# Optimization experiments

Measured on AMD Instinct MI355X. Metric: run time of the kernel, lower is better.

The kernel has to match this reference:

```python
import jax, jax.numpy as jnp
import numpy as np

B, T, D = 4, 2048, 2048
P, K, ALPHA, R = 512, 16, 4, 32
E_RATIO = 0.8
EPS = 1e-6


def rmsnorm(x, g):
    return x * jax.lax.rsqrt(jnp.mean(x * x, axis=-1, keepdims=True) + EPS) * g


def dale_signs():
    # first e_ratio*P neurons excitatory (+1), rest inhibitory (-1)
    return jnp.where(jnp.arange(P) < int(E_RATIO * P), 1.0, -1.0)


def quant_dale(w, signs):
    # STE sign-quantization with per-neuron mean-abs scale + Dale's-law sign constraint
    scale = jnp.mean(jnp.abs(w), axis=-1, keepdims=True)  # [P,1]
    q = scale * signs[:, None] * jnp.ones_like(w)         # magnitude=scale, sign fixed per neuron
    return w + jax.lax.stop_gradient(q - w)


def synapse_graph(x, idx, w):
    # x: [B,T,D], idx: [P,K] int, w: [P,K] -> dendritic inputs [B,T,P,K]
    return jnp.take(x, idx, axis=-1) * w


def perceptron(x_dend, Wp, Wout, signs):
    Wq = quant_dale(Wp, signs)                              # [P,K]
    u = jnp.einsum('btpk,pk->btp', x_dend, Wq)              # [B,T,P]
    f = jax.nn.sigmoid(u)                                   # gate [B,T,P]
    f_out = quant_dale(Wout, signs)                         # [P,ALPHA]
    y = (f * u)[..., None] * f_out                          # [B,T,P,ALPHA]
    return u, f, y, f_out


def low_rank_ssm(t, f, s0, U, V, Wgate, bgate):
    # t,f: [B,T,P]; s0: [B,R]. Low-rank gated linear scan in R dims.
    z = jnp.einsum('btp,pr->btr', t, U)
    lam = jax.nn.sigmoid(jnp.einsum('btp,pr->btr', f, Wgate) + bgate)

    def step(s, inp):
        z_t, l_t = inp
        s = l_t * s + z_t
        return s, s

    sT, S = jax.lax.scan(step, s0, (jnp.moveaxis(z, 1, 0), jnp.moveaxis(lam, 1, 0)))
    tilde = jnp.einsum('btr,rp->btp', jnp.moveaxis(S, 0, 1), V)
    return tilde, sT


def flatten_ports(y):
    return y.reshape(*y.shape[:-2], P * ALPHA)


def setup_inputs() -> dict:
    key = jax.random.key(0)
    ks = jax.random.split(key, 14)
    sc = 0.1
    return {
        'x': jax.random.normal(ks[0], (B, T, D), jnp.float32),
        'state': jnp.zeros((B, R), jnp.float32),
        'g1': jnp.ones((D,), jnp.float32),
        'g2': jnp.ones((D,), jnp.float32),
        'idx_ssm': jax.random.randint(ks[1], (P, K), 0, D),
        'wg_ssm': jax.random.normal(ks[2], (P, K), jnp.float32) * sc,
        'idx_mlp': jax.random.randint(ks[3], (P, K), 0, D),
        'wg_mlp': jax.random.normal(ks[4], (P, K), jnp.float32) * sc,
        'Wp_ssm': jax.random.normal(ks[5], (P, K), jnp.float32) * sc,
        'Wout_ssm': jax.random.normal(ks[6], (P, ALPHA), jnp.float32) * sc,
        'Wp_mlp': jax.random.normal(ks[7], (P, K), jnp.float32) * sc,
        'Wout_mlp': jax.random.normal(ks[8], (P, ALPHA), jnp.float32) * sc,
        'U': jax.random.normal(ks[9], (P, R), jnp.float32) * sc,
        'V': jax.random.normal(ks[10], (R, P), jnp.float32) * sc,
        'Wgate': jax.random.normal(ks[11], (P, R), jnp.float32) * sc,
        'bgate': jnp.zeros((R,), jnp.float32),
    }


def reference(x, state, g1, g2, idx_ssm, wg_ssm, idx_mlp, wg_mlp,
              Wp_ssm, Wout_ssm, Wp_mlp, Wout_mlp, U, V, Wgate, bgate):
    signs = dale_signs()
    # --- SSM branch ---
    h1 = rmsnorm(x, g1)
    x_dend_ssm = synapse_graph(h1, idx_ssm, wg_ssm)
    u_ssm, f_ssm, _, f_out = perceptron(x_dend_ssm, Wp_ssm, Wout_ssm, signs)
    t_ssm = f_ssm * u_ssm
    tilde_t, new_state = low_rank_ssm(t_ssm, f_ssm, state, U, V, Wgate, bgate)
    y_ssm = (f_ssm * tilde_t)[..., None] * f_out            # [B,T,P,ALPHA]
    x_after = x + flatten_ports(y_ssm)
    # --- MLP branch ---
    h2 = rmsnorm(x_after, g2)
    x_dend_mlp = synapse_graph(h2, idx_mlp, wg_mlp)
    _, _, y_mlp, _ = perceptron(x_dend_mlp, Wp_mlp, Wout_mlp, signs)
    x_out = x_after + flatten_ports(y_mlp)
    return x_out, new_state
```

## Files before the change

### kernel.cpp

```cpp
#include <hip/hip_runtime.h>
#include <hip/hip_bf16.h>

#define B_ 4
#define T_ 2048
#define D_ 2048
#define P_ 512
#define K_ 16
#define ALPHA_ 4
#define R_ 32
#define NE_ 409
#define EPS_ 1e-6f
#define G_ 4

typedef unsigned short u16;
typedef unsigned int u32;

__device__ __forceinline__ float sigmoidf_(float x) {
  return 1.0f / (1.0f + __expf(-x));
}
__device__ __forceinline__ float bfb2f(u32 u) {
  return __uint_as_float(u << 16);
}
__device__ __forceinline__ u16 f2bfb(float f) {
  __hip_bfloat16 h = __float2bfloat16(f);
  return *reinterpret_cast<u16*>(&h);
}

__global__ __launch_bounds__(256, 4) void k_phase1(
    const float* __restrict__ x, const float* __restrict__ g1,
    const int* __restrict__ idx, const float* __restrict__ wg,
    const float* __restrict__ U, const float* __restrict__ Wgt,
    const float* __restrict__ bg, const float* __restrict__ Wp,
    u16* __restrict__ f_ssm, float* __restrict__ z, float* __restrict__ lam) {
  __shared__ u16 h1[G_][D_];
  __shared__ u32 ft[G_][P_];
  __shared__ float red[G_][4];
  __shared__ float zp[G_][R_][4];
  __shared__ float lp[G_][R_][4];

  int tid = threadIdx.x;
  int token0 = blockIdx.x * G_;
  int b = token0 >> 11;
  int t0 = token0 & (T_ - 1);
  int p0 = 2 * tid, p1 = p0 + 1;

  float xv[G_][8];
#pragma unroll
  for (int tok = 0; tok < G_; tok++) {
    const float4* xp = reinterpret_cast<const float4*>(x + (size_t)(token0 + tok) * D_ + tid * 8);
    *reinterpret_cast<float4*>(&xv[tok][0]) = xp[0];
    *reinterpret_cast<float4*>(&xv[tok][4]) = xp[1];
  }
  float gv[8];
  {
    const float4* gp = reinterpret_cast<const float4*>(g1 + tid * 8);
    *reinterpret_cast<float4*>(&gv[0]) = gp[0];
    *reinterpret_cast<float4*>(&gv[4]) = gp[1];
  }
  float wq0, wq1;
  {
    const float4* w0 = reinterpret_cast<const float4*>(Wp + p0 * K_);
    const float4* w1 = reinterpret_cast<const float4*>(Wp + p1 * K_);
    float a0 = 0, a1 = 0;
#pragma unroll
    for (int q = 0; q < 4; q++) {
      float4 v0 = w0[q], v1 = w1[q];
      a0 += fabsf(v0.x) + fabsf(v0.y) + fabsf(v0.z) + fabsf(v0.w);
      a1 += fabsf(v1.x) + fabsf(v1.y) + fabsf(v1.z) + fabsf(v1.w);
    }
    wq0 = ((p0 < NE_) ? 1.0f : -1.0f) * a0 * (1.0f / K_);
    wq1 = ((p1 < NE_) ? 1.0f : -1.0f) * a1 * (1.0f / K_);
  }

#pragma unroll
  for (int tok = 0; tok < G_; tok++) {
    float s = 0;
#pragma unroll
    for (int i = 0; i < 8; i++) s += xv[tok][i] * xv[tok][i];
#pragma unroll
    for (int off = 32; off; off >>= 1) s += __shfl_down(s, off);
    if ((tid & 63) == 0) red[tok][tid >> 6] = s;
  }
  __syncthreads();
#pragma unroll
  for (int tok = 0; tok < G_; tok++) {
    float inv = rsqrtf((red[tok][0] + red[tok][1] + red[tok][2] + red[tok][3]) * (1.0f / D_) + EPS_);
    u16 tmp[8];
#pragma unroll
    for (int i = 0; i < 8; i++) tmp[i] = f2bfb(xv[tok][i] * inv * gv[i]);
    *reinterpret_cast<uint4*>(&h1[tok][tid * 8]) = *reinterpret_cast<const uint4*>(tmp);
  }

  union { int4 v[4]; int s[16]; } iu0, iu1;
  union { float4 v[4]; float s[16]; } wu0, wu1;
  {
    const int4* ip0 = reinterpret_cast<const int4*>(idx + p0 * K_);
    const int4* ip1 = reinterpret_cast<const int4*>(idx + p1 * K_);
    const float4* wp0 = reinterpret_cast<const float4*>(wg + p0 * K_);
    const float4* wp1 = reinterpret_cast<const float4*>(wg + p1 * K_);
#pragma unroll
    for (int q = 0; q < 4; q++) { iu0.v[q] = ip0[q]; iu1.v[q] = ip1[q]; wu0.v[q] = wp0[q]; wu1.v[q] = wp1[q]; }
  }
  __syncthreads();

#pragma unroll
  for (int tok = 0; tok < G_; tok++) {
    float a0 = 0, a1 = 0;
#pragma unroll
    for (int k = 0; k < K_; k++) {
      a0 += bfb2f(h1[tok][iu0.s[k]]) * wu0.s[k];
      a1 += bfb2f(h1[tok][iu1.s[k]]) * wu1.s[k];
    }
    float u0 = wq0 * a0, u1 = wq1 * a1;
    float f0 = sigmoidf_(u0), f1 = sigmoidf_(u1);
    u32 pk0 = (u32)f2bfb(f0) | ((u32)f2bfb(f0 * u0) << 16);
    u32 pk1 = (u32)f2bfb(f1) | ((u32)f2bfb(f1 * u1) << 16);
    *reinterpret_cast<uint2*>(&ft[tok][p0]) = make_uint2(pk0, pk1);
    *reinterpret_cast<u32*>(f_ssm + (size_t)(token0 + tok) * P_ + p0) =
        (u32)f2bfb(f0) | ((u32)f2bfb(f1) << 16);
  }
  __syncthreads();

  int r = tid & 31, g = tid >> 5;
  float zs[G_], ls[G_];
#pragma unroll
  for (int tok = 0; tok < G_; tok++) { zs[tok] = 0; ls[tok] = 0; }
  int pbase = g * 64;
#pragma unroll 8
  for (int pp = 0; pp < 64; pp++) {
    int p = pbase + pp;
    float uu = U[p * R_ + r];
    float ww = Wgt[p * R_ + r];
#pragma unroll
    for (int tok = 0; tok < G_; tok++) {
      u32 v = ft[tok][p];
      zs[tok] += bfb2f(v >> 16) * uu;
      ls[tok] += bfb2f(v & 0xffffu) * ww;
    }
  }
#pragma unroll
  for (int tok = 0; tok < G_; tok++) {
    zs[tok] += __shfl_down(zs[tok], 32);
    ls[tok] += __shfl_down(ls[tok], 32);
  }
  int wid = tid >> 6;
  if ((tid & 63) < 32) {
#pragma unroll
    for (int tok = 0; tok < G_; tok++) {
      zp[tok][r][wid] = zs[tok];
      lp[tok][r][wid] = ls[tok];
    }
  }
  __syncthreads();
  if (tid < R_) {
    float bgr = bg[tid];
    float z4[G_], l4[G_];
#pragma unroll
    for (int tok = 0; tok < G_; tok++) {
      float zz = zp[tok][tid][0] + zp[tok][tid][1] + zp[tok][tid][2] + zp[tok][tid][3];
      float ll = lp[tok][tid][0] + lp[tok][tid][1] + lp[tok][tid][2] + lp[tok][tid][3];
      z4[tok] = zz;
      l4[tok] = sigmoidf_(ll + bgr);
    }
    size_t o = ((size_t)(b * R_ + tid)) * T_ + t0;
    *reinterpret_cast<float4*>(&z[o]) = *reinterpret_cast<const float4*>(z4);
    *reinterpret_cast<float4*>(&lam[o]) = *reinterpret_cast<const float4*>(l4);
  }
}

__global__ __launch_bounds__(64) void k_scan(
    const float* __restrict__ z, const float* __restrict__ lam,
    const float* __restrict__ state, float* __restrict__ S,
    float* __restrict__ out_state) {
  int br = blockIdx.x;
  int lane = threadIdx.x;
  const float* zr = z + (size_t)br * T_ + lane * 32;
  const float* lr = lam + (size_t)br * T_ + lane * 32;
  float zb[32], lb[32];
#pragma unroll
  for (int i = 0; i < 32; i += 4) {
    *reinterpret_cast<float4*>(&zb[i]) = *reinterpret_cast<const float4*>(&zr[i]);
    *reinterpret_cast<float4*>(&lb[i]) = *reinterpret_cast<const float4*>(&lr[i]);
  }
  float A = 1.0f, Z = 0.0f;
#pragma unroll
  for (int i = 0; i < 32; i++) { Z = lb[i] * Z + zb[i]; A *= lb[i]; }
  for (int off = 1; off < 64; off <<= 1) {
    float Ap = __shfl_up(A, off);
    float Zp = __shfl_up(Z, off);
    if (lane >= off) { Z = A * Zp + Z; A = A * Ap; }
  }
  float s0 = state[br];
  float Ae = __shfl_up(A, 1);
  float Ze = __shfl_up(Z, 1);
  float s = (lane == 0) ? s0 : (Ae * s0 + Ze);
  float sb[32];
#pragma unroll
  for (int i = 0; i < 32; i++) { s = lb[i] * s + zb[i]; sb[i] = s; }
  float* Sr = S + (size_t)br * T_ + lane * 32;
#pragma unroll
  for (int i = 0; i < 32; i += 4)
    *reinterpret_cast<float4*>(&Sr[i]) = *reinterpret_cast<const float4*>(&sb[i]);
  if (lane == 63) out_state[br] = s;
}

__global__ __launch_bounds__(256, 4) void k_phase3(
    const float* __restrict__ x, const float* __restrict__ g2,
    const int* __restrict__ idx, const float* __restrict__ wg,
    const float* __restrict__ V, const float* __restrict__ S,
    const u16* __restrict__ f_ssm, const float* __restrict__ Wo_s,
    const float* __restrict__ Wp_m, const float* __restrict__ Wo_m,
    float* __restrict__ out) {
  __shared__ float Sl[G_][R_];
  __shared__ u16 h2[G_][D_];
  __shared__ float red[G_][4];

  int tid = threadIdx.x;
  int token0 = blockIdx.x * G_;
  int b = token0 >> 11;
  int t0 = token0 & (T_ - 1);
  int p0 = 2 * tid, p1 = p0 + 1;

  if (tid < G_ * R_) {
    int tok = tid >> 5, r = tid & 31;
    Sl[tok][r] = S[((size_t)(b * R_ + r)) * T_ + t0 + tok];
  }

  float xa[G_][8];
#pragma unroll
  for (int tok = 0; tok < G_; tok++) {
    const float4* xp = reinterpret_cast<const float4*>(x + (size_t)(token0 + tok) * D_ + tid * 8);
    *reinterpret_cast<float4*>(&xa[tok][0]) = xp[0];
    *reinterpret_cast<float4*>(&xa[tok][4]) = xp[1];
  }
  u32 fpair[G_];
#pragma unroll
  for (int tok = 0; tok < G_; tok++)
    fpair[tok] = *reinterpret_cast<const u32*>(f_ssm + (size_t)(token0 + tok) * P_ + p0);

  float sgn0 = (p0 < NE_) ? 1.0f : -1.0f;
  float sgn1 = (p1 < NE_) ? 1.0f : -1.0f;
  float fo_s0, fo_s1, fo_m0, fo_m1, wq_m0, wq_m1;
  {
    float4 a = *reinterpret_cast<const float4*>(Wo_s + p0 * ALPHA_);
    float4 c = *reinterpret_cast<const float4*>(Wo_s + p1 * ALPHA_);
    fo_s0 = sgn0 * (fabsf(a.x) + fabsf(a.y) + fabsf(a.z) + fabsf(a.w)) * (1.0f / ALPHA_);
    fo_s1 = sgn1 * (fabsf(c.x) + fabsf(c.y) + fabsf(c.z) + fabsf(c.w)) * (1.0f / ALPHA_);
    float4 e = *reinterpret_cast<const float4*>(Wo_m + p0 * ALPHA_);
    float4 g = *reinterpret_cast<const float4*>(Wo_m + p1 * ALPHA_);
    fo_m0 = sgn0 * (fabsf(e.x) + fabsf(e.y) + fabsf(e.z) + fabsf(e.w)) * (1.0f / ALPHA_);
    fo_m1 = sgn1 * (fabsf(g.x) + fabsf(g.y) + fabsf(g.z) + fabsf(g.w)) * (1.0f / ALPHA_);
    const float4* w0 = reinterpret_cast<const float4*>(Wp_m + p0 * K_);
    const float4* w1 = reinterpret_cast<const float4*>(Wp_m + p1 * K_);
    float a0 = 0, a1 = 0;
#pragma unroll
    for (int q = 0; q < 4; q++) {
      float4 v0 = w0[q], v1 = w1[q];
      a0 += fabsf(v0.x) + fabsf(v0.y) + fabsf(v0.z) + fabsf(v0.w);
      a1 += fabsf(v1.x) + fabsf(v1.y) + fabsf(v1.z) + fabsf(v1.w);
    }
    wq_m0 = sgn0 * a0 * (1.0f / K_);
    wq_m1 = sgn1 * a1 * (1.0f / K_);
  }
  float gv[8];
  {
    const float4* gp = reinterpret_cast<const float4*>(g2 + tid * 8);
    *reinterpret_cast<float4*>(&gv[0]) = gp[0];
    *reinterpret_cast<float4*>(&gv[4]) = gp[1];
  }
  __syncthreads();

  float til0[G_], til1[G_];
#pragma unroll
  for (int tok = 0; tok < G_; tok++) { til0[tok] = 0; til1[tok] = 0; }
#pragma unroll 8
  for (int r = 0; r < R_; r++) {
    float2 vv = *reinterpret_cast<const float2*>(V + r * P_ + p0);
#pragma unroll
    for (int tok = 0; tok < G_; tok++) {
      float s = Sl[tok][r];
      til0[tok] += s * vv.x;
      til1[tok] += s * vv.y;
    }
  }

#pragma unroll
  for (int tok = 0; tok < G_; tok++) {
    float f0 = bfb2f(fpair[tok] & 0xffffu);
    float f1 = bfb2f(fpair[tok] >> 16);
    float val0 = f0 * til0[tok] * fo_s0;
    float val1 = f1 * til1[tok] * fo_s1;
    float ss = 0;
#pragma unroll
    for (int a = 0; a < 4; a++) {
      xa[tok][a] += val0;
      xa[tok][4 + a] += val1;
      ss += xa[tok][a] * xa[tok][a] + xa[tok][4 + a] * xa[tok][4 + a];
    }
#pragma unroll
    for (int off = 32; off; off >>= 1) ss += __shfl_down(ss, off);
    if ((tid & 63) == 0) red[tok][tid >> 6] = ss;
  }
  __syncthreads();
#pragma unroll
  for (int tok = 0; tok < G_; tok++) {
    float inv = rsqrtf((red[tok][0] + red[tok][1] + red[tok][2] + red[tok][3]) * (1.0f / D_) + EPS_);
    u16 tmp[8];
#pragma unroll
    for (int i = 0; i < 8; i++) tmp[i] = f2bfb(xa[tok][i] * inv * gv[i]);
    *reinterpret_cast<uint4*>(&h2[tok][tid * 8]) = *reinterpret_cast<const uint4*>(tmp);
  }
  __syncthreads();

#pragma unroll
  for (int j = 0; j < 2; j++) {
    int p = p0 + j;
    union { int4 v[4]; int s[16]; } iu;
    union { float4 v[4]; float s[16]; } wu;
    const int4* ip = reinterpret_cast<const int4*>(idx + p * K_);
    const float4* wp = reinterpret_cast<const float4*>(wg + p * K_);
#pragma unroll
    for (int q = 0; q < 4; q++) { iu.v[q] = ip[q]; wu.v[q] = wp[q]; }
    float wqm = j ? wq_m1 : wq_m0;
    float fom = j ? fo_m1 : fo_m0;
#pragma unroll
    for (int tok = 0; tok < G_; tok++) {
      float acc = 0;
#pragma unroll
      for (int k = 0; k < K_; k++) acc += bfb2f(h2[tok][iu.s[k]]) * wu.s[k];
      float u = wqm * acc;
      float f = sigmoidf_(u);
      float val = f * u * fom;
#pragma unroll
      for (int a = 0; a < 4; a++) xa[tok][j * 4 + a] += val;
    }
  }
#pragma unroll
  for (int tok = 0; tok < G_; tok++) {
    float4* op = reinterpret_cast<float4*>(out + (size_t)(token0 + tok) * D_ + tid * 8);
    op[0] = *reinterpret_cast<const float4*>(&xa[tok][0]);
    op[1] = *reinterpret_cast<const float4*>(&xa[tok][4]);
  }
}

extern "C" void kernel_launch(void* const* d_in, const int* in_sizes, int n_in,
                              void* d_out, int out_size, void* d_ws, size_t ws_size,
                              hipStream_t stream) {
  const float* x     = (const float*)d_in[0];
  const float* state = (const float*)d_in[1];
  const float* g1    = (const float*)d_in[2];
  const float* g2    = (const float*)d_in[3];
  const int*   idx_s = (const int*)d_in[4];
  const float* wg_s  = (const float*)d_in[5];
  const int*   idx_m = (const int*)d_in[6];
  const float* wg_m  = (const float*)d_in[7];
  const float* Wp_s  = (const float*)d_in[8];
  const float* Wo_s  = (const float*)d_in[9];
  const float* Wp_m  = (const float*)d_in[10];
  const float* Wo_m  = (const float*)d_in[11];
  const float* U     = (const float*)d_in[12];
  const float* V     = (const float*)d_in[13];
  const float* Wgt   = (const float*)d_in[14];
  const float* bg    = (const float*)d_in[15];
  float* out = (float*)d_out;

  char* ws = (char*)d_ws;
  u16* f_ssm = (u16*)ws;
  size_t off = (size_t)B_ * T_ * P_ * 2;
  float* z   = (float*)(ws + off); off += (size_t)B_ * R_ * T_ * 4;
  float* lam = (float*)(ws + off); off += (size_t)B_ * R_ * T_ * 4;
  float* S   = (float*)(ws + off);

  hipLaunchKernelGGL(k_phase1, dim3(B_ * T_ / G_), dim3(256), 0, stream,
                     x, g1, idx_s, wg_s, U, Wgt, bg, Wp_s, f_ssm, z, lam);
  hipLaunchKernelGGL(k_scan, dim3(B_ * R_), dim3(64), 0, stream,
                     z, lam, state, S, out + (size_t)B_ * T_ * D_);
  hipLaunchKernelGGL(k_phase3, dim3(B_ * T_ / G_), dim3(256), 0, stream,
                     x, g2, idx_m, wg_m, V, S, f_ssm, Wo_s, Wp_m, Wo_m, out);
}
```

Measured before the change: 254.4 us.

## Fuse three kernels into one cooperative persistent kernel with grid syncs

Replaces the three separate launches (phase1, scan, phase3) with a single cooperative kernel that loops over token groups persistently and uses grid.sync between phases, falling back to the three-kernel path if the cooperative launch fails. The aim is to remove launch gaps and tail effects between phases. It also hand-rolls the bf16 rounding, moves the idx/wg loads before a sync, and merges phase3's two per-neuron gather loops into one. The risks are grid-wide barrier cost, the scan phase using only 128 blocks while the rest idle, and occupancy limits of the persistent grid.

```diff
diff --git a/kernel.cpp b/kernel.cpp
--- a/kernel.cpp
+++ b/kernel.cpp
@@ -1,5 +1,8 @@
 #include <hip/hip_runtime.h>
 #include <hip/hip_bf16.h>
+#include <hip/hip_cooperative_groups.h>
+
+namespace cg = cooperative_groups;
 
 #define B_ 4
 #define T_ 2048
@@ -11,6 +14,7 @@
 #define NE_ 409
 #define EPS_ 1e-6f
 #define G_ 4
+#define NGRP_ (B_ * T_ / G_)
 
 typedef unsigned short u16;
 typedef unsigned int u32;
@@ -22,45 +26,80 @@
   return __uint_as_float(u << 16);
 }
 __device__ __forceinline__ u16 f2bfb(float f) {
-  __hip_bfloat16 h = __float2bfloat16(f);
-  return *reinterpret_cast<u16*>(&h);
-}
-
-__global__ __launch_bounds__(256, 4) void k_phase1(
+  u32 bits = __float_as_uint(f);
+  u32 lsb = (bits >> 16) & 1u;
+  bits += 0x7fffu + lsb;
+  return (u16)(bits >> 16);
+}
+
+struct SmemP1 {
+  u16 h[G_ * D_];
+  u32 ftw[G_ * P_];
+  float zp[G_][R_][4];
+  float lp[G_][R_][4];
+  float red[G_][4];
+};
+struct SmemP3 {
+  u16 h[G_ * D_];
+  float Sl[G_][R_];
+  float red[G_][4];
+};
+union SmemU { SmemP1 p1; SmemP3 p3; };
+
+__device__ __forceinline__ void phase1_dev(
+    SmemP1& sm, int gi, int tid,
     const float* __restrict__ x, const float* __restrict__ g1,
-    const int* __restrict__ idx, const float* __restrict__ wg,
-    const float* __restrict__ U, const float* __restrict__ Wgt,
-    const float* __restrict__ bg, const float* __restrict__ Wp,
-    u16* __restrict__ f_ssm, float* __restrict__ z, float* __restrict__ lam) {
-  __shared__ u16 h1[G_][D_];
-  __shared__ u32 ft[G_][P_];
-  __shared__ float red[G_][4];
-  __shared__ float zp[G_][R_][4];
-  __shared__ float lp[G_][R_][4];
-
-  int tid = threadIdx.x;
-  int token0 = blockIdx.x * G_;
+    const int* __restrict__ idx_s, const float* __restrict__ wg_s,
+    const float* __restrict__ Wp_s, const float* __restrict__ U,
+    const float* __restrict__ Wgt, const float* __restrict__ bg,
+    u32* __restrict__ ftg, float* __restrict__ z, float* __restrict__ lam) {
+  int token0 = gi * G_;
   int b = token0 >> 11;
   int t0 = token0 & (T_ - 1);
   int p0 = 2 * tid, p1 = p0 + 1;
 
+  float gv[8];
+  {
+    const float4* gp = reinterpret_cast<const float4*>(g1 + tid * 8);
+    *reinterpret_cast<float4*>(&gv[0]) = gp[0];
+    *reinterpret_cast<float4*>(&gv[4]) = gp[1];
+  }
   float xv[G_][8];
 #pragma unroll
   for (int tok = 0; tok < G_; tok++) {
     const float4* xp = reinterpret_cast<const float4*>(x + (size_t)(token0 + tok) * D_ + tid * 8);
     *reinterpret_cast<float4*>(&xv[tok][0]) = xp[0];
     *reinterpret_cast<float4*>(&xv[tok][4]) = xp[1];
-  }
-  float gv[8];
-  {
-    const float4* gp = reinterpret_cast<const float4*>(g1 + tid * 8);
-    *reinterpret_cast<float4*>(&gv[0]) = gp[0];
-    *reinterpret_cast<float4*>(&gv[4]) = gp[1];
+    float ss = 0;
+#pragma unroll
+    for (int i = 0; i < 8; i++) ss += xv[tok][i] * xv[tok][i];
+#pragma unroll
+    for (int off = 32; off; off >>= 1) ss += __shfl_down(ss, off);
+    if ((tid & 63) == 0) sm.red[tok][tid >> 6] = ss;
+  }
+  __syncthreads();
+#pragma unroll
+  for (int tok = 0; tok < G_; tok++) {
+    float inv = rsqrtf((sm.red[tok][0] + sm.red[tok][1] + sm.red[tok][2] + sm.red[tok][3]) * (1.0f / D_) + EPS_);
+    u16 tmp[8];
+#pragma unroll
+    for (int i = 0; i < 8; i++) tmp[i] = f2bfb(xv[tok][i] * inv * gv[i]);
+    *reinterpret_cast<uint4*>(&sm.h[tok * D_ + tid * 8]) = *reinterpret_cast<const uint4*>(tmp);
+  }
+  union { int4 v[4]; int s[16]; } iu0, iu1;
+  union { float4 v[4]; float s[16]; } wu0, wu1;
+  {
+    const int4* ip0 = reinterpret_cast<const int4*>(idx_s + p0 * K_);
+    const int4* ip1 = reinterpret_cast<const int4*>(idx_s + p1 * K_);
+    const float4* wp0 = reinterpret_cast<const float4*>(wg_s + p0 * K_);
+    const float4* wp1 = reinterpret_cast<const float4*>(wg_s + p1 * K_);
+#pragma unroll
+    for (int q = 0; q < 4; q++) { iu0.v[q] = ip0[q]; iu1.v[q] = ip1[q]; wu0.v[q] = wp0[q]; wu1.v[q] = wp1[q]; }
   }
   float wq0, wq1;
   {
-    const float4* w0 = reinterpret_cast<const float4*>(Wp + p0 * K_);
-    const float4* w1 = reinterpret_cast<const float4*>(Wp + p1 * K_);
+    const float4* w0 = reinterpret_cast<const float4*>(Wp_s + p0 * K_);
+    const float4* w1 = reinterpret_cast<const float4*>(Wp_s + p1 * K_);
     float a0 = 0, a1 = 0;
 #pragma unroll
     for (int q = 0; q < 4; q++) {
@@ -71,36 +110,6 @@
     wq0 = ((p0 < NE_) ? 1.0f : -1.0f) * a0 * (1.0f / K_);
     wq1 = ((p1 < NE_) ? 1.0f : -1.0f) * a1 * (1.0f / K_);
   }
-
-#pragma unroll
-  for (int tok = 0; tok < G_; tok++) {
-    float s = 0;
-#pragma unroll
-    for (int i = 0; i < 8; i++) s += xv[tok][i] * xv[tok][i];
-#pragma unroll
-    for (int off = 32; off; off >>= 1) s += __shfl_down(s, off);
-    if ((tid & 63) == 0) red[tok][tid >> 6] = s;
-  }
-  __syncthreads();
-#pragma unroll
-  for (int tok = 0; tok < G_; tok++) {
-    float inv = rsqrtf((red[tok][0] + red[tok][1] + red[tok][2] + red[tok][3]) * (1.0f / D_) + EPS_);
-    u16 tmp[8];
-#pragma unroll
-    for (int i = 0; i < 8; i++) tmp[i] = f2bfb(xv[tok][i] * inv * gv[i]);
-    *reinterpret_cast<uint4*>(&h1[tok][tid * 8]) = *reinterpret_cast<const uint4*>(tmp);
-  }
-
-  union { int4 v[4]; int s[16]; } iu0, iu1;
-  union { float4 v[4]; float s[16]; } wu0, wu1;
-  {
-    const int4* ip0 = reinterpret_cast<const int4*>(idx + p0 * K_);
-    const int4* ip1 = reinterpret_cast<const int4*>(idx + p1 * K_);
-    const float4* wp0 = reinterpret_cast<const float4*>(wg + p0 * K_);
-    const float4* wp1 = reinterpret_cast<const float4*>(wg + p1 * K_);
-#pragma unroll
-    for (int q = 0; q < 4; q++) { iu0.v[q] = ip0[q]; iu1.v[q] = ip1[q]; wu0.v[q] = wp0[q]; wu1.v[q] = wp1[q]; }
-  }
   __syncthreads();
 
 #pragma unroll
@@ -108,24 +117,23 @@
     float a0 = 0, a1 = 0;
 #pragma unroll
     for (int k = 0; k < K_; k++) {
-      a0 += bfb2f(h1[tok][iu0.s[k]]) * wu0.s[k];
-      a1 += bfb2f(h1[tok][iu1.s[k]]) * wu1.s[k];
+      a0 += bfb2f(sm.h[tok * D_ + iu0.s[k]]) * wu0.s[k];
+      a1 += bfb2f(sm.h[tok * D_ + iu1.s[k]]) * wu1.s[k];
     }
     float u0 = wq0 * a0, u1 = wq1 * a1;
     float f0 = sigmoidf_(u0), f1 = sigmoidf_(u1);
     u32 pk0 = (u32)f2bfb(f0) | ((u32)f2bfb(f0 * u0) << 16);
     u32 pk1 = (u32)f2bfb(f1) | ((u32)f2bfb(f1 * u1) << 16);
-    *reinterpret_cast<uint2*>(&ft[tok][p0]) = make_uint2(pk0, pk1);
-    *reinterpret_cast<u32*>(f_ssm + (size_t)(token0 + tok) * P_ + p0) =
-        (u32)f2bfb(f0) | ((u32)f2bfb(f1) << 16);
-  }
-  __syncthreads();
-
-  int r = tid & 31, g = tid >> 5;
+    *reinterpret_cast<uint2*>(&sm.ftw[tok * P_ + p0]) = make_uint2(pk0, pk1);
+    ftg[(size_t)(token0 + tok) * 256 + tid] = (u32)f2bfb(f0) | ((u32)f2bfb(f1) << 16);
+  }
+  __syncthreads();
+
+  int r = tid & 31, grp = tid >> 5;
   float zs[G_], ls[G_];
 #pragma unroll
   for (int tok = 0; tok < G_; tok++) { zs[tok] = 0; ls[tok] = 0; }
-  int pbase = g * 64;
+  int pbase = grp * 64;
 #pragma unroll 8
   for (int pp = 0; pp < 64; pp++) {
     int p = pbase + pp;
@@ -133,7 +141,7 @@
     float ww = Wgt[p * R_ + r];
 #pragma unroll
     for (int tok = 0; tok < G_; tok++) {
-      u32 v = ft[tok][p];
+      u32 v = sm.ftw[tok * P_ + p];
       zs[tok] += bfb2f(v >> 16) * uu;
       ls[tok] += bfb2f(v & 0xffffu) * ww;
     }
@@ -147,8 +155,8 @@
   if ((tid & 63) < 32) {
 #pragma unroll
     for (int tok = 0; tok < G_; tok++) {
-      zp[tok][r][wid] = zs[tok];
-      lp[tok][r][wid] = ls[tok];
+      sm.zp[tok][r][wid] = zs[tok];
+      sm.lp[tok][r][wid] = ls[tok];
     }
   }
   __syncthreads();
@@ -157,8 +165,8 @@
     float z4[G_], l4[G_];
 #pragma unroll
     for (int tok = 0; tok < G_; tok++) {
-      float zz = zp[tok][tid][0] + zp[tok][tid][1] + zp[tok][tid][2] + zp[tok][tid][3];
-      float ll = lp[tok][tid][0] + lp[tok][tid][1] + lp[tok][tid][2] + lp[tok][tid][3];
+      float zz = sm.zp[tok][tid][0] + sm.zp[tok][tid][1] + sm.zp[tok][tid][2] + sm.zp[tok][tid][3];
+      float ll = sm.lp[tok][tid][0] + sm.lp[tok][tid][1] + sm.lp[tok][tid][2] + sm.lp[tok][tid][3];
       z4[tok] = zz;
       l4[tok] = sigmoidf_(ll + bgr);
     }
@@ -166,14 +174,16 @@
     *reinterpret_cast<float4*>(&z[o]) = *reinterpret_cast<const float4*>(z4);
     *reinterpret_cast<float4*>(&lam[o]) = *reinterpret_cast<const float4*>(l4);
   }
-}
-
-__global__ __launch_bounds__(64) void k_scan(
+  __syncthreads();
+}
+
+__device__ __forceinline__ void scan_dev(
+    int br, int tid,
     const float* __restrict__ z, const float* __restrict__ lam,
     const float* __restrict__ state, float* __restrict__ S,
     float* __restrict__ out_state) {
-  int br = blockIdx.x;
-  int lane = threadIdx.x;
+  if (tid >= 64) return;
+  int lane = tid;
   const float* zr = z + (size_t)br * T_ + lane * 32;
   const float* lr = lam + (size_t)br * T_ + lane * 32;
   float zb[32], lb[32];
@@ -204,52 +214,36 @@
   if (lane == 63) out_state[br] = s;
 }
 
-__global__ __launch_bounds__(256, 4) void k_phase3(
+__device__ __forceinline__ void phase3_dev(
+    SmemP3& sm, int gi, int tid,
     const float* __restrict__ x, const float* __restrict__ g2,
-    const int* __restrict__ idx, const float* __restrict__ wg,
-    const float* __restrict__ V, const float* __restrict__ S,
-    const u16* __restrict__ f_ssm, const float* __restrict__ Wo_s,
-    const float* __restrict__ Wp_m, const float* __restrict__ Wo_m,
+    const int* __restrict__ idx_m, const float* __restrict__ wg_m,
+    const float* __restrict__ Wo_s, const float* __restrict__ Wp_m,
+    const float* __restrict__ Wo_m, const float* __restrict__ V,
+    const float* __restrict__ S, const u32* __restrict__ ftg,
     float* __restrict__ out) {
-  __shared__ float Sl[G_][R_];
-  __shared__ u16 h2[G_][D_];
-  __shared__ float red[G_][4];
-
-  int tid = threadIdx.x;
-  int token0 = blockIdx.x * G_;
+  int token0 = gi * G_;
   int b = token0 >> 11;
   int t0 = token0 & (T_ - 1);
   int p0 = 2 * tid, p1 = p0 + 1;
 
   if (tid < G_ * R_) {
-    int tok = tid >> 5, r = tid & 31;
-    Sl[tok][r] = S[((size_t)(b * R_ + r)) * T_ + t0 + tok];
-  }
-
-  float xa[G_][8];
-#pragma unroll
-  for (int tok = 0; tok < G_; tok++) {
-    const float4* xp = reinterpret_cast<const float4*>(x + (size_t)(token0 + tok) * D_ + tid * 8);
-    *reinterpret_cast<float4*>(&xa[tok][0]) = xp[0];
-    *reinterpret_cast<float4*>(&xa[tok][4]) = xp[1];
-  }
-  u32 fpair[G_];
-#pragma unroll
-  for (int tok = 0; tok < G_; tok++)
-    fpair[tok] = *reinterpret_cast<const u32*>(f_ssm + (size_t)(token0 + tok) * P_ + p0);
+    int tok = tid >> 5, rr = tid & 31;
+    sm.Sl[tok][rr] = S[((size_t)(b * R_ + rr)) * T_ + t0 + tok];
+  }
 
   float sgn0 = (p0 < NE_) ? 1.0f : -1.0f;
   float sgn1 = (p1 < NE_) ? 1.0f : -1.0f;
   float fo_s0, fo_s1, fo_m0, fo_m1, wq_m0, wq_m1;
   {
-    float4 a = *reinterpret_cast<const float4*>(Wo_s + p0 * ALPHA_);
-    float4 c = *reinterpret_cast<const float4*>(Wo_s + p1 * ALPHA_);
-    fo_s0 = sgn0 * (fabsf(a.x) + fabsf(a.y) + fabsf(a.z) + fabsf(a.w)) * (1.0f / ALPHA_);
-    fo_s1 = sgn1 * (fabsf(c.x) + fabsf(c.y) + fabsf(c.z) + fabsf(c.w)) * (1.0f / ALPHA_);
-    float4 e = *reinterpret_cast<const float4*>(Wo_m + p0 * ALPHA_);
-    float4 g = *reinterpret_cast<const float4*>(Wo_m + p1 * ALPHA_);
-    fo_m0 = sgn0 * (fabsf(e.x) + fabsf(e.y) + fabsf(e.z) + fabsf(e.w)) * (1.0f / ALPHA_);
-    fo_m1 = sgn1 * (fabsf(g.x) + fabsf(g.y) + fabsf(g.z) + fabsf(g.w)) * (1.0f / ALPHA_);
+    float4 c0 = *reinterpret_cast<const float4*>(Wo_s + p0 * ALPHA_);
+    float4 c1 = *reinterpret_cast<const float4*>(Wo_s + p1 * ALPHA_);
+    float4 d0 = *reinterpret_cast<const float4*>(Wo_m + p0 * ALPHA_);
+    float4 d1 = *reinterpret_cast<const float4*>(Wo_m + p1 * ALPHA_);
+    fo_s0 = sgn0 * (fabsf(c0.x) + fabsf(c0.y) + fabsf(c0.z) + fabsf(c0.w)) * (1.0f / ALPHA_);
+    fo_s1 = sgn1 * (fabsf(c1.x) + fabsf(c1.y) + fabsf(c1.z) + fabsf(c1.w)) * (1.0f / ALPHA_);
+    fo_m0 = sgn0 * (fabsf(d0.x) + fabsf(d0.y) + fabsf(d0.z) + fabsf(d0.w)) * (1.0f / ALPHA_);
+    fo_m1 = sgn1 * (fabsf(d1.x) + fabsf(d1.y) + fabsf(d1.z) + fabsf(d1.w)) * (1.0f / ALPHA_);
     const float4* w0 = reinterpret_cast<const float4*>(Wp_m + p0 * K_);
     const float4* w1 = reinterpret_cast<const float4*>(Wp_m + p1 * K_);
     float a0 = 0, a1 = 0;
@@ -274,73 +268,134 @@
 #pragma unroll
   for (int tok = 0; tok < G_; tok++) { til0[tok] = 0; til1[tok] = 0; }
 #pragma unroll 8
-  for (int r = 0; r < R_; r++) {
-    float2 vv = *reinterpret_cast<const float2*>(V + r * P_ + p0);
+  for (int rr = 0; rr < R_; rr++) {
+    float2 vv = *reinterpret_cast<const float2*>(V + rr * P_ + p0);
 #pragma unroll
     for (int tok = 0; tok < G_; tok++) {
-      float s = Sl[tok][r];
+      float s = sm.Sl[tok][rr];
       til0[tok] += s * vv.x;
       til1[tok] += s * vv.y;
     }
   }
 
-#pragma unroll
-  for (int tok = 0; tok < G_; tok++) {
-    float f0 = bfb2f(fpair[tok] & 0xffffu);
-    float f1 = bfb2f(fpair[tok] >> 16);
+  float xa[G_][8];
+#pragma unroll
+  for (int tok = 0; tok < G_; tok++) {
+    size_t trow = (size_t)(token0 + tok);
+    const float4* xp = reinterpret_cast<const float4*>(x + trow * D_ + tid * 8);
+    float xvv[8];
+    *reinterpret_cast<float4*>(&xvv[0]) = xp[0];
+    *reinterpret_cast<float4*>(&xvv[4]) = xp[1];
+    u32 fp = ftg[trow * 256 + tid];
+    float f0 = bfb2f(fp & 0xffffu);
+    float f1 = bfb2f(fp >> 16);
     float val0 = f0 * til0[tok] * fo_s0;
     float val1 = f1 * til1[tok] * fo_s1;
     float ss = 0;
 #pragma unroll
     for (int a = 0; a < 4; a++) {
-      xa[tok][a] += val0;
-      xa[tok][4 + a] += val1;
-      ss += xa[tok][a] * xa[tok][a] + xa[tok][4 + a] * xa[tok][4 + a];
+      float v0 = xvv[a] + val0;
+      float v1 = xvv[4 + a] + val1;
+      xa[tok][a] = v0;
+      xa[tok][4 + a] = v1;
+      ss += v0 * v0 + v1 * v1;
     }
 #pragma unroll
     for (int off = 32; off; off >>= 1) ss += __shfl_down(ss, off);
-    if ((tid & 63) == 0) red[tok][tid >> 6] = ss;
-  }
-  __syncthreads();
-#pragma unroll
-  for (int tok = 0; tok < G_; tok++) {
-    float inv = rsqrtf((red[tok][0] + red[tok][1] + red[tok][2] + red[tok][3]) * (1.0f / D_) + EPS_);
+    if ((tid & 63) == 0) sm.red[tok][tid >> 6] = ss;
+  }
+  __syncthreads();
+#pragma unroll
+  for (int tok = 0; tok < G_; tok++) {
+    float inv = rsqrtf((sm.red[tok][0] + sm.red[tok][1] + sm.red[tok][2] + sm.red[tok][3]) * (1.0f / D_) + EPS_);
     u16 tmp[8];
 #pragma unroll
     for (int i = 0; i < 8; i++) tmp[i] = f2bfb(xa[tok][i] * inv * gv[i]);
-    *reinterpret_cast<uint4*>(&h2[tok][tid * 8]) = *reinterpret_cast<const uint4*>(tmp);
-  }
-  __syncthreads();
-
-#pragma unroll
-  for (int j = 0; j < 2; j++) {
-    int p = p0 + j;
-    union { int4 v[4]; int s[16]; } iu;
-    union { float4 v[4]; float s[16]; } wu;
-    const int4* ip = reinterpret_cast<const int4*>(idx + p * K_);
-    const float4* wp = reinterpret_cast<const float4*>(wg + p * K_);
-#pragma unroll
-    for (int q = 0; q < 4; q++) { iu.v[q] = ip[q]; wu.v[q] = wp[q]; }
-    float wqm = j ? wq_m1 : wq_m0;
-    float fom = j ? fo_m1 : fo_m0;
-#pragma unroll
-    for (int tok = 0; tok < G_; tok++) {
-      float acc = 0;
-#pragma unroll
-      for (int k = 0; k < K_; k++) acc += bfb2f(h2[tok][iu.s[k]]) * wu.s[k];
-      float u = wqm * acc;
-      float f = sigmoidf_(u);
-      float val = f * u * fom;
-#pragma unroll
-      for (int a = 0; a < 4; a++) xa[tok][j * 4 + a] += val;
-    }
-  }
-#pragma unroll
-  for (int tok = 0; tok < G_; tok++) {
+    *reinterpret_cast<uint4*>(&sm.h[tok * D_ + tid * 8]) = *reinterpret_cast<const uint4*>(tmp);
+  }
+  union { int4 v[4]; int s[16]; } iu0, iu1;
+  union { float4 v[4]; float s[16]; } wu0, wu1;
+  {
+    const int4* ip0 = reinterpret_cast<const int4*>(idx_m + p0 * K_);
+    const int4* ip1 = reinterpret_cast<const int4*>(idx_m + p1 * K_);
+    const float4* wp0 = reinterpret_cast<const float4*>(wg_m + p0 * K_);
+    const float4* wp1 = reinterpret_cast<const float4*>(wg_m + p1 * K_);
+#pragma unroll
+    for (int q = 0; q < 4; q++) { iu0.v[q] = ip0[q]; iu1.v[q] = ip1[q]; wu0.v[q] = wp0[q]; wu1.v[q] = wp1[q]; }
+  }
+  __syncthreads();
+
+#pragma unroll
+  for (int tok = 0; tok < G_; tok++) {
+    float a0 = 0, a1 = 0;
+#pragma unroll
+    for (int k = 0; k < K_; k++) {
+      a0 += bfb2f(sm.h[tok * D_ + iu0.s[k]]) * wu0.s[k];
+      a1 += bfb2f(sm.h[tok * D_ + iu1.s[k]]) * wu1.s[k];
+    }
+    float u0 = wq_m0 * a0, u1 = wq_m1 * a1;
+    float f0 = sigmoidf_(u0), f1 = sigmoidf_(u1);
+    float val0 = f0 * u0 * fo_m0, val1 = f1 * u1 * fo_m1;
+    float ov[8];
+#pragma unroll
+    for (int a = 0; a < 4; a++) {
+      ov[a] = xa[tok][a] + val0;
+      ov[4 + a] = xa[tok][4 + a] + val1;
+    }
     float4* op = reinterpret_cast<float4*>(out + (size_t)(token0 + tok) * D_ + tid * 8);
-    op[0] = *reinterpret_cast<const float4*>(&xa[tok][0]);
-    op[1] = *reinterpret_cast<const float4*>(&xa[tok][4]);
-  }
+    op[0] = *reinterpret_cast<const float4*>(&ov[0]);
+    op[1] = *reinterpret_cast<const float4*>(&ov[4]);
+  }
+  __syncthreads();
+}
+
+__global__ __launch_bounds__(256, 4) void k_fused(
+    const float* __restrict__ x, const float* __restrict__ g1,
+    const float* __restrict__ g2,
+    const int* __restrict__ idx_s, const float* __restrict__ wg_s,
+    const int* __restrict__ idx_m, const float* __restrict__ wg_m,
+    const float* __restrict__ Wp_s, const float* __restrict__ Wo_s,
+    const float* __restrict__ Wp_m, const float* __restrict__ Wo_m,
+    const float* __restrict__ U, const float* __restrict__ V,
+    const float* __restrict__ Wgt, const float* __restrict__ bg,
+    const float* __restrict__ state,
+    u32* __restrict__ ftg, float* __restrict__ z, float* __restrict__ lam,
+    float* __restrict__ S, float* __restrict__ out, float* __restrict__ out_state) {
+  __shared__ SmemU sm;
+  cg::grid_group grid = cg::this_grid();
+  int tid = threadIdx.x;
+
+  for (int gi = blockIdx.x; gi < NGRP_; gi += gridDim.x)
+    phase1_dev(sm.p1, gi, tid, x, g1, idx_s, wg_s, Wp_s, U, Wgt, bg, ftg, z, lam);
+
+  grid.sync();
+
+  for (int br = blockIdx.x; br < B_ * R_; br += gridDim.x)
+    scan_dev(br, tid, z, lam, state, S, out_state);
+
+  grid.sync();
+
+  for (int gi = blockIdx.x; gi < NGRP_; gi += gridDim.x)
+    phase3_dev(sm.p3, gi, tid, x, g2, idx_m, wg_m, Wo_s, Wp_m, Wo_m, V, S, ftg, out);
+}
+
+__global__ __launch_bounds__(256) void k_p1(
+    const float* x, const float* g1, const int* idx_s, const float* wg_s,
+    const float* Wp_s, const float* U, const float* Wgt, const float* bg,
+    u32* ftg, float* z, float* lam) {
+  __shared__ SmemP1 sm;
+  phase1_dev(sm, blockIdx.x, threadIdx.x, x, g1, idx_s, wg_s, Wp_s, U, Wgt, bg, ftg, z, lam);
+}
+__global__ __launch_bounds__(64) void k_scan(
+    const float* z, const float* lam, const float* state, float* S, float* out_state) {
+  scan_dev(blockIdx.x, threadIdx.x, z, lam, state, S, out_state);
+}
+__global__ __launch_bounds__(256) void k_p3(
+    const float* x, const float* g2, const int* idx_m, const float* wg_m,
+    const float* Wo_s, const float* Wp_m, const float* Wo_m, const float* V,
+    const float* S, const u32* ftg, float* out) {
+  __shared__ SmemP3 sm;
+  phase3_dev(sm, blockIdx.x, threadIdx.x, x, g2, idx_m, wg_m, Wo_s, Wp_m, Wo_m, V, S, ftg, out);
 }
 
 extern "C" void kernel_launch(void* const* d_in, const int* in_sizes, int n_in,
@@ -363,18 +418,35 @@
   const float* Wgt   = (const float*)d_in[14];
   const float* bg    = (const float*)d_in[15];
   float* out = (float*)d_out;
+  float* out_state = out + (size_t)B_ * T_ * D_;
 
   char* ws = (char*)d_ws;
-  u16* f_ssm = (u16*)ws;
-  size_t off = (size_t)B_ * T_ * P_ * 2;
-  float* z   = (float*)(ws + off); off += (size_t)B_ * R_ * T_ * 4;
-  float* lam = (float*)(ws + off); off += (size_t)B_ * R_ * T_ * 4;
-  float* S   = (float*)(ws + off);
-
-  hipLaunchKernelGGL(k_phase1, dim3(B_ * T_ / G_), dim3(256), 0, stream,
-                     x, g1, idx_s, wg_s, U, Wgt, bg, Wp_s, f_ssm, z, lam);
-  hipLaunchKernelGGL(k_scan, dim3(B_ * R_), dim3(64), 0, stream,
-                     z, lam, state, S, out + (size_t)B_ * T_ * D_);
-  hipLaunchKernelGGL(k_phase3, dim3(B_ * T_ / G_), dim3(256), 0, stream,
-                     x, g2, idx_m, wg_m, V, S, f_ssm, Wo_s, Wp_m, Wo_m, out);
-}
+  float* z   = (float*)ws;
+  float* lam = (float*)(ws + (size_t)(1 << 20));
+  float* S   = (float*)(ws + (size_t)(2 << 20));
+  u32* ftg   = (u32*)(ws + (size_t)(3 << 20));
+
+  int occ = 0;
+  hipError_t qe = hipOccupancyMaxActiveBlocksPerMultiprocessor(&occ, k_fused, 256, 0);
+  int grid = (qe == hipSuccess && occ > 0) ? occ * 256 : 0;
+  if (grid > NGRP_) grid = NGRP_;
+
+  hipError_t le = hipErrorUnknown;
+  if (grid > 0) {
+    void* args[] = {
+        (void*)&x, (void*)&g1, (void*)&g2, (void*)&idx_s, (void*)&wg_s,
+        (void*)&idx_m, (void*)&wg_m, (void*)&Wp_s, (void*)&Wo_s,
+        (void*)&Wp_m, (void*)&Wo_m, (void*)&U, (void*)&V, (void*)&Wgt,
+        (void*)&bg, (void*)&state, (void*)&ftg, (void*)&z, (void*)&lam,
+        (void*)&S, (void*)&out, (void*)&out_state};
+    le = hipLaunchCooperativeKernel(k_fused, dim3(grid), dim3(256), args, 0, stream);
+  }
+  if (le != hipSuccess) {
+    hipLaunchKernelGGL(k_p1, dim3(NGRP_), dim3(256), 0, stream,
+                       x, g1, idx_s, wg_s, Wp_s, U, Wgt, bg, ftg, z, lam);
+    hipLaunchKernelGGL(k_scan, dim3(B_ * R_), dim3(64), 0, stream,
+                       z, lam, state, S, out_state);
+    hipLaunchKernelGGL(k_p3, dim3(NGRP_), dim3(256), 0, stream,
+                       x, g2, idx_m, wg_m, Wo_s, Wp_m, Wo_m, V, S, ftg, out);
+  }
+}
```

Result: slower. 550.0 us (+116.2%).
